# Optimization experiments

Measured on AMD Instinct MI355X. Metric: run time of the kernel, lower is better.

## Reference

```python
import jax, jax.numpy as jnp
import numpy as np

H = 4  # pairwise_num_attention_heads

def _layer_norm(x, gamma, beta, eps=1e-5):
    mu = jnp.mean(x, axis=-1, keepdims=True)
    var = jnp.var(x, axis=-1, keepdims=True)
    return (x - mu) * jax.lax.rsqrt(var + eps) * gamma + beta

def setup_inputs() -> dict:
    key = jax.random.key(0)
    ks = jax.random.split(key, 8)
    B, L, P = 1, 256, 128
    s = 0.02
    return {
        "pairwise_states": jax.random.normal(ks[0], (B, L, L, P), jnp.float32),
        "ln_gamma": jnp.ones((P,), jnp.float32),
        "ln_beta": jnp.zeros((P,), jnp.float32),
        "Wq": jax.random.normal(ks[1], (P, P), jnp.float32) * s,
        "Wk": jax.random.normal(ks[2], (P, P), jnp.float32) * s,
        "Wv": jax.random.normal(ks[3], (P, P), jnp.float32) * s,
        "Wb": jax.random.normal(ks[4], (P, H), jnp.float32) * s,
        "Wg": jax.random.normal(ks[5], (P, P), jnp.float32) * s,
        "bg": jnp.zeros((P,), jnp.float32),
        "Wo": jax.random.normal(ks[6], (P, P), jnp.float32) * s,
        "bo": jnp.zeros((P,), jnp.float32),
    }

def reference(pairwise_states, ln_gamma, ln_beta, Wq, Wk, Wv, Wb, Wg, bg, Wo, bo):
    # Row-axis triangle attention (RibonanzaNetPairwiseAttention, axis='row', eval mode).
    B, L, _, P = pairwise_states.shape
    D = P // H  # attention_head_size
    x = _layer_norm(pairwise_states, ln_gamma, ln_beta)  # [b,i,j,p]
    q = (x @ Wq).reshape(B, L, L, H, D)
    k = (x @ Wk).reshape(B, L, L, H, D)
    v = (x @ Wv).reshape(B, L, L, H, D)
    scale = jnp.asarray(D, x.dtype) ** 0.5
    # pairwise bias: [b,i,j,h] -> broadcast over the row axis of the scores
    bias = jnp.einsum('bijp,ph->bhij', x, Wb)  # [b,h,L,L]
    # scores[b,h,i,j,k]: within row i, query position j attends to key position k
    scores = jnp.einsum('bijhd,bikhd->bhijk', q, k) / scale + bias[:, :, None]
    probs = jax.nn.softmax(scores, axis=-1)
    ctx = jnp.einsum('bhijk,bikhd->bijhd', probs, v).reshape(B, L, L, P)
    gate = jax.nn.sigmoid(x @ Wg + bg)
    ctx = gate * ctx
    # output dense + residual (AxisDropout is identity in eval mode)
    return ctx @ Wo + bo + pairwise_states
```

## Files before the change

kernel.cpp:

```cpp
#include <hip/hip_runtime.h>

#define NPOS 65536

typedef __attribute__((ext_vector_type(8))) short bf16x8;
typedef __attribute__((ext_vector_type(4))) float f32x4;

#if __has_builtin(__builtin_amdgcn_exp2f)
#define EXP2F(x) __builtin_amdgcn_exp2f(x)
#else
#define EXP2F(x) __expf((x) * 0.6931471805599453f)
#endif
#if __has_builtin(__builtin_amdgcn_rcpf)
#define RCPF(x) __builtin_amdgcn_rcpf(x)
#else
#define RCPF(x) (1.0f / (x))
#endif

static __device__ __forceinline__ unsigned short f2bf(float f) {
  union { float f; unsigned int u; } v; v.f = f;
  unsigned int r = v.u + 0x7fffu + ((v.u >> 16) & 1u);
  return (unsigned short)(r >> 16);
}
static __device__ __forceinline__ float lo_bf(unsigned int u) {
  union { unsigned int u; float f; } v; v.u = u << 16; return v.f;
}
static __device__ __forceinline__ float hi_bf(unsigned int u) {
  union { unsigned int u; float f; } v; v.u = u & 0xffff0000u; return v.f;
}
static __device__ __forceinline__ unsigned int permpack(float hi, float lo) {
  union { float f; unsigned int u; } a, b;
  a.f = hi; b.f = lo;
#if __has_builtin(__builtin_amdgcn_perm)
  return __builtin_amdgcn_perm(a.u, b.u, 0x07060302u);
#else
  return (a.u & 0xffff0000u) | (b.u >> 16);
#endif
}

__global__ void k_pack(const float* __restrict__ Wq, const float* __restrict__ Wk,
                       const float* __restrict__ Wv, const float* __restrict__ Wg,
                       const float* __restrict__ Wo,
                       ushort* __restrict__ WT, ushort* __restrict__ WoT) {
  int idx = blockIdx.x * blockDim.x + threadIdx.x;
  if (idx < 512 * 128) {
    int n = idx >> 7, k = idx & 127;
    int nn = n & 127;
    float val;
    if (n < 128)      val = Wq[k * 128 + nn] * (0.17677669529663687f * 1.4426950408889634f);
    else if (n < 256) val = Wk[k * 128 + nn];
    else if (n < 384) val = Wv[k * 128 + nn];
    else              val = Wg[k * 128 + nn];
    WT[idx] = f2bf(val);
  } else if (idx < 512 * 128 + 128 * 128) {
    int j = idx - 512 * 128;
    int n = j >> 7, k = j & 127;
    WoT[j] = f2bf(Wo[k * 128 + n]);
  }
}

__global__ __launch_bounds__(128, 4) void k_ln(
    const float* __restrict__ in, const float* __restrict__ gamma,
    const float* __restrict__ beta, const float* __restrict__ Wb,
    ushort* __restrict__ xln, ushort* __restrict__ biasB) {
  int t = threadIdx.x, wv = t >> 6, lane = t & 63;
  int n = lane & 15, g = lane >> 4;
  int myrow = blockIdx.x * 32 + wv * 16 + n;
  const float* rp = in + (size_t)myrow * 128;

  float xv[32];
  float sm = 0.f, ssm = 0.f;
  #pragma unroll
  for (int kc = 0; kc < 4; kc++)
    #pragma unroll
    for (int pr = 0; pr < 2; pr++) {
      float4 v = *(const float4*)(rp + kc * 32 + g * 8 + pr * 4);
      int o = kc * 8 + pr * 4;
      xv[o] = v.x; xv[o+1] = v.y; xv[o+2] = v.z; xv[o+3] = v.w;
      sm  += v.x + v.y + v.z + v.w;
      ssm += v.x*v.x + v.y*v.y + v.z*v.z + v.w*v.w;
    }
  sm  += __shfl_xor(sm, 16, 64);  sm  += __shfl_xor(sm, 32, 64);
  ssm += __shfl_xor(ssm, 16, 64); ssm += __shfl_xor(ssm, 32, 64);
  float mu  = sm * (1.0f / 128.0f);
  float var = ssm * (1.0f / 128.0f) - mu * mu;
  float rs  = rsqrtf(var + 1e-5f);
  float p0 = 0.f, p1 = 0.f, p2 = 0.f, p3 = 0.f;
  #pragma unroll
  for (int kc = 0; kc < 4; kc++)
    #pragma unroll
    for (int pr = 0; pr < 2; pr++) {
      int c0 = kc * 32 + g * 8 + pr * 4;
      float4 g4 = *(const float4*)(gamma + c0);
      float4 b4 = *(const float4*)(beta + c0);
      int o = kc * 8 + pr * 4;
      #pragma unroll
      for (int r = 0; r < 4; r++) {
        float xn = (xv[o + r] - mu) * rs * (&g4.x)[r] + (&b4.x)[r];
        xv[o + r] = xn;
        float4 w = ((const float4*)Wb)[c0 + r];
        p0 += xn * w.x; p1 += xn * w.y; p2 += xn * w.z; p3 += xn * w.w;
      }
    }
  #pragma unroll
  for (int kc = 0; kc < 4; kc++)
    #pragma unroll
    for (int pr = 0; pr < 2; pr++) {
      int o = kc * 8 + pr * 4;
      uint2 px;
      px.x = (unsigned int)f2bf(xv[o]) | ((unsigned int)f2bf(xv[o + 1]) << 16);
      px.y = (unsigned int)f2bf(xv[o + 2]) | ((unsigned int)f2bf(xv[o + 3]) << 16);
      *(uint2*)(xln + (size_t)myrow * 128 + kc * 32 + g * 8 + pr * 4) = px;
    }
  p0 += __shfl_xor(p0, 16, 64); p0 += __shfl_xor(p0, 32, 64);
  p1 += __shfl_xor(p1, 16, 64); p1 += __shfl_xor(p1, 32, 64);
  p2 += __shfl_xor(p2, 16, 64); p2 += __shfl_xor(p2, 32, 64);
  p3 += __shfl_xor(p3, 16, 64); p3 += __shfl_xor(p3, 32, 64);
  if (g == 0) {
    const float l2e = 1.4426950408889634f;
    biasB[0 * NPOS + myrow] = f2bf(p0 * l2e);
    biasB[1 * NPOS + myrow] = f2bf(p1 * l2e);
    biasB[2 * NPOS + myrow] = f2bf(p2 * l2e);
    biasB[3 * NPOS + myrow] = f2bf(p3 * l2e);
  }
}

#define KS 40
#define VS 264
#define QS 40
__global__ __launch_bounds__(512, 2) void k_attn2(
    const ushort* __restrict__ xln, const ushort* __restrict__ WT,
    const float* __restrict__ bg, const ushort* __restrict__ biasB,
    ushort* __restrict__ gctx) {
  __shared__ __align__(16) ushort Klds[256 * KS];
  __shared__ __align__(16) ushort VTlds[32 * VS];
  __shared__ __align__(16) ushort qstg[8][32 * QS];
  int i = blockIdx.x & 255, h = blockIdx.x >> 8;
  int t = threadIdx.x, wv = t >> 6, lane = t & 63;
  int n = lane & 15, g = lane >> 4;
  int r0 = wv * 32;

  bf16x8 a[2][4];
  const ushort* xb = xln + ((size_t)i * 256 + r0) * 128;
  #pragma unroll
  for (int c = 0; c < 2; c++)
    #pragma unroll
    for (int kc = 0; kc < 4; kc++)
      a[c][kc] = *(const bf16x8*)(xb + (size_t)(c * 16 + n) * 128 + kc * 32 + g * 8);

  f32x4 gs[2][2];
  #pragma unroll
  for (int sect = 0; sect < 4; sect++) {
    bf16x8 b[2][4];
    #pragma unroll
    for (int ntl = 0; ntl < 2; ntl++)
      #pragma unroll
      for (int kc = 0; kc < 4; kc++)
        b[ntl][kc] = *(const bf16x8*)(WT + (size_t)(sect * 128 + h * 32 + ntl * 16 + n) * 128 + kc * 32 + g * 8);
    #pragma unroll
    for (int c = 0; c < 2; c++) {
      f32x4 acc[2];
      #pragma unroll
      for (int ntl = 0; ntl < 2; ntl++) {
        f32x4 cc = {0.f, 0.f, 0.f, 0.f};
        #pragma unroll
        for (int kc = 0; kc < 4; kc++)
          cc = __builtin_amdgcn_mfma_f32_16x16x32_bf16(a[c][kc], b[ntl][kc], cc, 0, 0, 0);
        acc[ntl] = cc;
      }
      if (sect == 0) {
        #pragma unroll
        for (int ntl = 0; ntl < 2; ntl++)
          #pragma unroll
          for (int r = 0; r < 4; r++)
            qstg[wv][(c * 16 + g * 4 + r) * QS + ntl * 16 + n] = f2bf(acc[ntl][r]);
      } else if (sect == 1) {
        #pragma unroll
        for (int ntl = 0; ntl < 2; ntl++)
          #pragma unroll
          for (int r = 0; r < 4; r++)
            Klds[(r0 + c * 16 + g * 4 + r) * KS + ntl * 16 + n] = f2bf(acc[ntl][r]);
      } else if (sect == 2) {
        #pragma unroll
        for (int ntl = 0; ntl < 2; ntl++) {
          uint2 vp;
          vp.x = (unsigned int)f2bf(acc[ntl][0]) | ((unsigned int)f2bf(acc[ntl][1]) << 16);
          vp.y = (unsigned int)f2bf(acc[ntl][2]) | ((unsigned int)f2bf(acc[ntl][3]) << 16);
          *(uint2*)(&VTlds[(ntl * 16 + n) * VS + r0 + c * 16 + g * 4]) = vp;
        }
      } else {
        #pragma unroll
        for (int ntl = 0; ntl < 2; ntl++)
          #pragma unroll
          for (int r = 0; r < 4; r++)
            gs[c][ntl][r] = 1.0f / (1.0f + __expf(-(acc[ntl][r] + bg[h * 32 + ntl * 16 + n])));
      }
    }
  }
  __syncthreads();

  const ushort* bb = biasB + (size_t)h * NPOS;
  #pragma unroll
  for (int tt = 0; tt < 2; tt++) {
    int j0 = r0 + tt * 16;
    bf16x8 bq = *(const bf16x8*)(&qstg[wv][(tt * 16 + n) * QS + g * 8]);
    uint2 bv[16];
    #pragma unroll
    for (int kt = 0; kt < 16; kt++)
      bv[kt] = *(const uint2*)(bb + (size_t)(j0 + n) * 256 + kt * 16 + g * 4);
    f32x4 s[16];
    #pragma unroll
    for (int kt = 0; kt < 16; kt++) {
      bf16x8 ak = *(const bf16x8*)(&Klds[(kt * 16 + n) * KS + g * 8]);
      f32x4 cc;
      cc[0] = lo_bf(bv[kt].x); cc[1] = hi_bf(bv[kt].x);
      cc[2] = lo_bf(bv[kt].y); cc[3] = hi_bf(bv[kt].y);
      s[kt] = __builtin_amdgcn_mfma_f32_16x16x32_bf16(ak, bq, cc, 0, 0, 0);
    }
    f32x4 a4 = {0.f, 0.f, 0.f, 0.f};
    #pragma unroll
    for (int kt = 0; kt < 16; kt++) {
      #pragma unroll
      for (int r = 0; r < 4; r++) s[kt][r] = EXP2F(s[kt][r]);
      a4 += s[kt];
    }
    float smm = (a4[0] + a4[1]) + (a4[2] + a4[3]);
    smm += __shfl_xor(smm, 16, 64);
    smm += __shfl_xor(smm, 32, 64);
    float inv = RCPF(smm);
    f32x4 ctx0 = {0.f, 0.f, 0.f, 0.f}, ctx1 = {0.f, 0.f, 0.f, 0.f};
    #pragma unroll
    for (int c8 = 0; c8 < 8; c8++) {
      union { bf16x8 v; uint2 u[2]; } ap;
      ap.u[0].x = permpack(s[c8*2][1] * inv, s[c8*2][0] * inv);
      ap.u[0].y = permpack(s[c8*2][3] * inv, s[c8*2][2] * inv);
      ap.u[1].x = permpack(s[c8*2+1][1] * inv, s[c8*2+1][0] * inv);
      ap.u[1].y = permpack(s[c8*2+1][3] * inv, s[c8*2+1][2] * inv);
      union { bf16x8 v; uint2 u[2]; } v0, v1;
      v0.u[0] = *(const uint2*)(&VTlds[(size_t)n * VS + c8 * 32 + g * 4]);
      v0.u[1] = *(const uint2*)(&VTlds[(size_t)n * VS + c8 * 32 + 16 + g * 4]);
      v1.u[0] = *(const uint2*)(&VTlds[(size_t)(16 + n) * VS + c8 * 32 + g * 4]);
      v1.u[1] = *(const uint2*)(&VTlds[(size_t)(16 + n) * VS + c8 * 32 + 16 + g * 4]);
      ctx0 = __builtin_amdgcn_mfma_f32_16x16x32_bf16(ap.v, v0.v, ctx0, 0, 0, 0);
      ctx1 = __builtin_amdgcn_mfma_f32_16x16x32_bf16(ap.v, v1.v, ctx1, 0, 0, 0);
    }
    #pragma unroll
    for (int r = 0; r < 4; r++) {
      size_t pos = (size_t)i * 256 + j0 + g * 4 + r;
      gctx[pos * 128 + h * 32 + n]      = f2bf(ctx0[r] * gs[tt][0][r]);
      gctx[pos * 128 + h * 32 + 16 + n] = f2bf(ctx1[r] * gs[tt][1][r]);
    }
  }
}

__global__ __launch_bounds__(256, 4) void k_out(
    const ushort* __restrict__ gctx, const ushort* __restrict__ WoT,
    const float* __restrict__ bo, const float* __restrict__ in0,
    float* __restrict__ out) {
  int t = threadIdx.x, wv = t >> 6, lane = t & 63;
  int n = lane & 15, g = lane >> 4;
  int row0 = blockIdx.x * 64 + wv * 16;
  bf16x8 cfr[4];
  #pragma unroll
  for (int kc = 0; kc < 4; kc++)
    cfr[kc] = *(const bf16x8*)(gctx + (size_t)(row0 + n) * 128 + kc * 32 + g * 8);
  size_t rowg = (size_t)row0 + n;
  #pragma unroll
  for (int ntl = 0; ntl < 8; ntl++) {
    f32x4 acc = {0.f, 0.f, 0.f, 0.f};
    #pragma unroll
    for (int kc = 0; kc < 4; kc++) {
      bf16x8 wo = *(const bf16x8*)(WoT + (size_t)(ntl * 16 + n) * 128 + kc * 32 + g * 8);
      acc = __builtin_amdgcn_mfma_f32_16x16x32_bf16(wo, cfr[kc], acc, 0, 0, 0);
    }
    f32x4 b4 = *(const f32x4*)(bo + ntl * 16 + g * 4);
    size_t o = rowg * 128 + ntl * 16 + g * 4;
    f32x4 r4 = *(const f32x4*)(in0 + o);
    acc[0] += b4[0] + r4[0]; acc[1] += b4[1] + r4[1];
    acc[2] += b4[2] + r4[2]; acc[3] += b4[3] + r4[3];
    *(f32x4*)(out + o) = acc;
  }
}

extern "C" void kernel_launch(void* const* d_in, const int* in_sizes, int n_in,
                              void* d_out, int out_size, void* d_ws, size_t ws_size,
                              hipStream_t stream) {
  const float* in0   = (const float*)d_in[0];
  const float* gamma = (const float*)d_in[1];
  const float* beta  = (const float*)d_in[2];
  const float* Wq    = (const float*)d_in[3];
  const float* Wk    = (const float*)d_in[4];
  const float* Wv    = (const float*)d_in[5];
  const float* Wb    = (const float*)d_in[6];
  const float* Wg    = (const float*)d_in[7];
  const float* bg    = (const float*)d_in[8];
  const float* Wo    = (const float*)d_in[9];
  const float* bo    = (const float*)d_in[10];
  float* out = (float*)d_out;
  char* ws = (char*)d_ws;

  const size_t MB = 1024 * 1024;
  ushort* gctx  = (ushort*)(ws);
  ushort* xln   = (ushort*)(ws + 16 * MB);
  ushort* biasB = (ushort*)(ws + 32 * MB);
  ushort* WT    = (ushort*)(ws + 33 * MB);
  ushort* WoT   = (ushort*)(ws + 33 * MB + 128 * 1024);

  k_pack <<<320, 256, 0, stream>>>(Wq, Wk, Wv, Wg, Wo, WT, WoT);
  k_ln   <<<2048, 128, 0, stream>>>(in0, gamma, beta, Wb, xln, biasB);
  k_attn2<<<1024, 512, 0, stream>>>(xln, WT, bg, biasB, gctx);
  k_out  <<<1024, 256, 0, stream>>>(gctx, WoT, bo, in0, out);
}
```

Baseline: 217.2 us.

## Stage softmax probs through LDS for contiguous V loads and raise occupancy

Probabilities are now written to a per-wave LDS scratch (reusing the Q staging buffer) and read back in the MFMA A-operand layout. This lets V fragments be loaded as single contiguous 16-byte reads instead of split 8-byte pieces. K and Q LDS row strides shrink from 40 to 36, with the loads split into 8-byte halves to keep alignment, and the launch bound asks for 3 blocks per CU. The aim is less LDS footprint and higher occupancy, at the cost of extra LDS writes and reads for P and possible bank conflicts or register spills under the tighter bound.

```diff
diff --git a/kernel.cpp b/kernel.cpp
--- a/kernel.cpp
+++ b/kernel.cpp
@@ -124,10 +124,10 @@
   }
 }
 
-#define KS 40
+#define KS 36
 #define VS 264
-#define QS 40
-__global__ __launch_bounds__(512, 2) void k_attn2(
+#define QS 36
+__global__ __launch_bounds__(512, 3) void k_attn2(
     const ushort* __restrict__ xln, const ushort* __restrict__ WT,
     const float* __restrict__ bg, const ushort* __restrict__ biasB,
     ushort* __restrict__ gctx) {
@@ -202,7 +202,10 @@
   #pragma unroll
   for (int tt = 0; tt < 2; tt++) {
     int j0 = r0 + tt * 16;
-    bf16x8 bq = *(const bf16x8*)(&qstg[wv][(tt * 16 + n) * QS + g * 8]);
+    union { bf16x8 v; uint2 u[2]; } bq;
+    bq.u[0] = *(const uint2*)(&qstg[wv][(tt * 16 + n) * QS + g * 8]);
+    bq.u[1] = *(const uint2*)(&qstg[wv][(tt * 16 + n) * QS + g * 8 + 4]);
+    ushort* Pw = &qstg[wv][tt * 16 * QS];
     uint2 bv[16];
     #pragma unroll
     for (int kt = 0; kt < 16; kt++)
@@ -210,11 +213,13 @@
     f32x4 s[16];
     #pragma unroll
     for (int kt = 0; kt < 16; kt++) {
-      bf16x8 ak = *(const bf16x8*)(&Klds[(kt * 16 + n) * KS + g * 8]);
+      union { bf16x8 v; uint2 u[2]; } ak;
+      ak.u[0] = *(const uint2*)(&Klds[(kt * 16 + n) * KS + g * 8]);
+      ak.u[1] = *(const uint2*)(&Klds[(kt * 16 + n) * KS + g * 8 + 4]);
       f32x4 cc;
       cc[0] = lo_bf(bv[kt].x); cc[1] = hi_bf(bv[kt].x);
       cc[2] = lo_bf(bv[kt].y); cc[3] = hi_bf(bv[kt].y);
-      s[kt] = __builtin_amdgcn_mfma_f32_16x16x32_bf16(ak, bq, cc, 0, 0, 0);
+      s[kt] = __builtin_amdgcn_mfma_f32_16x16x32_bf16(ak.v, bq.v, cc, 0, 0, 0);
     }
     f32x4 a4 = {0.f, 0.f, 0.f, 0.f};
     #pragma unroll
@@ -230,18 +235,21 @@
     f32x4 ctx0 = {0.f, 0.f, 0.f, 0.f}, ctx1 = {0.f, 0.f, 0.f, 0.f};
     #pragma unroll
     for (int c8 = 0; c8 < 8; c8++) {
+      #pragma unroll
+      for (int t2 = 0; t2 < 2; t2++) {
+        int kt = c8 * 2 + t2;
+        uint2 pp;
+        pp.x = permpack(s[kt][1] * inv, s[kt][0] * inv);
+        pp.y = permpack(s[kt][3] * inv, s[kt][2] * inv);
+        *(uint2*)(&Pw[n * QS + t2 * 16 + g * 4]) = pp;
+      }
       union { bf16x8 v; uint2 u[2]; } ap;
-      ap.u[0].x = permpack(s[c8*2][1] * inv, s[c8*2][0] * inv);
-      ap.u[0].y = permpack(s[c8*2][3] * inv, s[c8*2][2] * inv);
-      ap.u[1].x = permpack(s[c8*2+1][1] * inv, s[c8*2+1][0] * inv);
-      ap.u[1].y = permpack(s[c8*2+1][3] * inv, s[c8*2+1][2] * inv);
-      union { bf16x8 v; uint2 u[2]; } v0, v1;
-      v0.u[0] = *(const uint2*)(&VTlds[(size_t)n * VS + c8 * 32 + g * 4]);
-      v0.u[1] = *(const uint2*)(&VTlds[(size_t)n * VS + c8 * 32 + 16 + g * 4]);
-      v1.u[0] = *(const uint2*)(&VTlds[(size_t)(16 + n) * VS + c8 * 32 + g * 4]);
-      v1.u[1] = *(const uint2*)(&VTlds[(size_t)(16 + n) * VS + c8 * 32 + 16 + g * 4]);
-      ctx0 = __builtin_amdgcn_mfma_f32_16x16x32_bf16(ap.v, v0.v, ctx0, 0, 0, 0);
-      ctx1 = __builtin_amdgcn_mfma_f32_16x16x32_bf16(ap.v, v1.v, ctx1, 0, 0, 0);
+      ap.u[0] = *(const uint2*)(&Pw[n * QS + g * 8]);
+      ap.u[1] = *(const uint2*)(&Pw[n * QS + g * 8 + 4]);
+      bf16x8 v0 = *(const bf16x8*)(&VTlds[(size_t)n * VS + c8 * 32 + g * 8]);
+      bf16x8 v1 = *(const bf16x8*)(&VTlds[(size_t)(16 + n) * VS + c8 * 32 + g * 8]);
+      ctx0 = __builtin_amdgcn_mfma_f32_16x16x32_bf16(ap.v, v0, ctx0, 0, 0, 0);
+      ctx1 = __builtin_amdgcn_mfma_f32_16x16x32_bf16(ap.v, v1, ctx1, 0, 0, 0);
     }
     #pragma unroll
     for (int r = 0; r < 4; r++) {
```

After: 242.9 us. 1.12x slower.
